# Kernel tuning notes

Hardware: AMD Instinct MI355X
Metric: run time of the kernel (lower is better)

## Reference

```python
import jax, jax.numpy as jnp
import numpy as np

VOCAB = 250002
UNUSED = np.array([0, 2, 1, 3])  # cls, eos, pad, unk token ids for XLM-R tokenizer
TEMP = 0.02
H = 1024


def _normalize(x, axis=-1):
    n = jnp.sqrt(jnp.sum(x * x, axis=axis, keepdims=True))
    return x / jnp.maximum(n, 1e-12)


def _sparse_embedding(hidden, ids, sparse_w, sparse_b):
    # token_weights = relu(Linear(H,1)(hidden)) -> [B, L]
    tw = jax.nn.relu(jnp.einsum('blh,h->bl', hidden, sparse_w) + sparse_b)
    B = hidden.shape[0]
    # torch: scatter into [B, L, V] then max over L; since tw >= 0 and base is 0,
    # this equals a scatter-max into [B, V] (avoids the huge [B,L,V] intermediate).
    emb = jnp.zeros((B, VOCAB), tw.dtype)
    emb = emb.at[jnp.arange(B)[:, None], ids].max(tw)
    emb = emb.at[:, UNUSED].set(0.0)
    return emb


def _colbert_embedding(hidden, mask, colbert_w, colbert_b):
    # Linear on tokens 1: (drop CLS), mask, then L2-normalize
    v = jnp.einsum('blh,dh->bld', hidden[:, 1:], colbert_w) + colbert_b
    v = v * mask[:, 1:, None]
    return _normalize(v)


def setup_inputs() -> dict:
    key = jax.random.key(0)
    ks = jax.random.split(key, 8)
    return {
        'q_hidden': jax.random.normal(ks[0], (8, 128, H), jnp.float32),
        'p_hidden': jax.random.normal(ks[1], (64, 512, H), jnp.float32),
        'q_mask': jnp.ones((8, 128), jnp.float32),
        'p_mask': jnp.ones((64, 512), jnp.float32),
        'q_ids': jax.random.randint(ks[2], (8, 128), 0, VOCAB),
        'p_ids': jax.random.randint(ks[3], (64, 512), 0, VOCAB),
        'colbert_w': jax.random.normal(ks[4], (H, H), jnp.float32) * 0.02,
        'colbert_b': jnp.zeros((H,), jnp.float32),
        'sparse_w': jax.random.normal(ks[5], (H,), jnp.float32) * 0.02,
        'sparse_b': jnp.zeros((), jnp.float32),
    }


def reference(q_hidden, p_hidden, q_mask, p_mask, q_ids, p_ids,
              colbert_w, colbert_b, sparse_w, sparse_b):
    # dense: cls pooling + normalize
    q_dense = _normalize(q_hidden[:, 0])
    p_dense = _normalize(p_hidden[:, 0])
    dense_scores = (q_dense @ p_dense.T) / TEMP  # [Bq, Bp]

    # sparse: relu-weighted vocab scatter-max
    q_sparse = _sparse_embedding(q_hidden, q_ids, sparse_w, sparse_b)
    p_sparse = _sparse_embedding(p_hidden, p_ids, sparse_w, sparse_b)
    sparse_scores = (q_sparse @ p_sparse.T) / TEMP  # [Bq, Bp]

    # colbert: late-interaction maxsim
    q_col = _colbert_embedding(q_hidden, q_mask, colbert_w, colbert_b)  # [Bq, Lq-1, H]
    p_col = _colbert_embedding(p_hidden, p_mask, colbert_w, colbert_b)  # [Bp, Lp-1, H]
    token_scores = jnp.einsum('qin,pjn->qipj', q_col, p_col)  # [Bq, Lq-1, Bp, Lp-1]
    colbert_scores = token_scores.max(-1).sum(1)
    colbert_scores = colbert_scores / q_mask[:, 1:].sum(-1, keepdims=True)
    colbert_scores = colbert_scores / TEMP  # [Bq, Bp]

    return dense_scores, sparse_scores, colbert_scores
```

## Files before the change

### kernel.cpp

```cpp
#include <hip/hip_runtime.h>
#include <hip/hip_bf16.h>


typedef __bf16 bf16x8 __attribute__((ext_vector_type(8)));
typedef float floatx4 __attribute__((ext_vector_type(4)));
typedef unsigned short ushort8v __attribute__((ext_vector_type(8)));

#define TEMP 0.02f

__device__ __forceinline__ unsigned short f2bf(float f) {
    unsigned u = __float_as_uint(f);
    unsigned r = (u + 0x7FFFu + ((u >> 16) & 1u)) >> 16;
    return (unsigned short)r;
}
__device__ __forceinline__ unsigned encf(float f) {
    unsigned u = __float_as_uint(f);
    return (u & 0x80000000u) ? ~u : (u | 0x80000000u);
}
__device__ __forceinline__ float decf(unsigned u) {
    return __uint_as_float((u & 0x80000000u) ? (u & 0x7FFFFFFFu) : ~u);
}

__device__ __forceinline__ void async_load16(void* lds, const void* g) {
    __builtin_amdgcn_global_load_lds(
        (__attribute__((address_space(1))) void*)g,
        (__attribute__((address_space(3))) void*)lds,
        16, 0, 0);
}

__global__ void conv_zero_tw(const float* __restrict__ qh, const float* __restrict__ ph,
                             const float* __restrict__ wsrc, unsigned short* __restrict__ dst,
                             const float* __restrict__ sw, const float* __restrict__ sb,
                             float* __restrict__ tw, unsigned* __restrict__ zbase)
{
    __shared__ float red[4];
    int b = blockIdx.x, t = threadIdx.x;
    if (b < 388) zbase[b * 256 + t] = 0u;
    int r0 = b * 2;
    const float* src;
    bool do_tw = true;
    if (r0 < 1024)       { src = qh   + (size_t)r0 * 1024; }
    else if (r0 < 33792) { src = ph   + (size_t)(r0 - 1024) * 1024; }
    else                 { src = wsrc + (size_t)(r0 - 33792) * 1024; do_tw = false; }
    const float4* s4 = (const float4*)src;
    float4 a = s4[t * 2], c = s4[t * 2 + 1];
    ushort8v o;
    o[0] = f2bf(a.x); o[1] = f2bf(a.y); o[2] = f2bf(a.z); o[3] = f2bf(a.w);
    o[4] = f2bf(c.x); o[5] = f2bf(c.y); o[6] = f2bf(c.z); o[7] = f2bf(c.w);
    ((ushort8v*)dst)[(size_t)b * 256 + t] = o;
    if (do_tw) {
        const float4* w4 = (const float4*)sw;
        int wi = (t & 127) * 2;
        float4 wa = w4[wi], wc = w4[wi + 1];
        float acc = a.x * wa.x + a.y * wa.y + a.z * wa.z + a.w * wa.w
                  + c.x * wc.x + c.y * wc.y + c.z * wc.z + c.w * wc.w;
        #pragma unroll
        for (int s = 32; s; s >>= 1) acc += __shfl_down(acc, s, 64);
        if ((t & 63) == 0) red[t >> 6] = acc;
        __syncthreads();
        if (t == 0)   tw[r0]     = fmaxf(red[0] + red[1] + sb[0], 0.0f);
        if (t == 128) tw[r0 + 1] = fmaxf(red[2] + red[3] + sb[0], 0.0f);
    }
}

__global__ void canon_all(const int* __restrict__ q_ids, const int* __restrict__ p_ids,
                          const float* __restrict__ tw,
                          float* __restrict__ eff_q, float* __restrict__ eff_p)
{
    __shared__ int   sid[512];
    __shared__ float stw[512];
    int b = blockIdx.x, t = threadIdx.x;
    const int* ids; const float* twr; float* eff; int L, chunk;
    if (b < 8) {
        L = 128; chunk = 0;
        ids = q_ids + b * 128; twr = tw + b * 128; eff = eff_q + b * 128;
    } else {
        int pr = (b - 8) >> 1; chunk = (b - 8) & 1; L = 512;
        ids = p_ids + pr * 512; twr = tw + 1024 + pr * 512; eff = eff_p + pr * 512;
    }
    for (int l = t; l < L; l += 256) { sid[l] = ids[l]; stw[l] = twr[l]; }
    __syncthreads();
    int l = chunk * 256 + t;
    if (l < L) {
        int id = sid[l];
        float wv = stw[l];
        bool kill = (id < 4);
        #pragma unroll 8
        for (int m = 0; m < L; ++m) {
            int idm = sid[m];
            float wm = stw[m];
            bool beats = (idm == id) & (m != l) & ((wm > wv) | ((wm == wv) & (m < l)));
            kill = kill | beats;
        }
        eff[l] = kill ? 0.0f : wv;
    }
}

template<int MODE>
__global__ __launch_bounds__(256, 2)
void gemm_bt(const unsigned short* __restrict__ A,
             const unsigned short* __restrict__ B,
             const float* __restrict__ bias,
             unsigned short* __restrict__ C,
             unsigned* __restrict__ Mbuf,
             float* __restrict__ normsq,
             const float* __restrict__ p_mask,
             int nTails, int N, int K,
             const float* __restrict__ qh, const float* __restrict__ ph,
             const int* __restrict__ q_ids, const int* __restrict__ p_ids,
             const float* __restrict__ eff_q, const float* __restrict__ eff_p,
             float* __restrict__ out)
{
    __shared__ unsigned short smA[128 * 64];
    __shared__ unsigned short smB[128 * 64];
    const int tid  = threadIdx.x;

    if (MODE == 0 && (int)blockIdx.x < nTails) {
        int pair = (int)blockIdx.x;
        int qb = pair >> 6, pb = pair & 63;
        char* lds = (char*)smA;
        int*   qid = (int*)lds;
        float* qef = (float*)(lds + 512);
        int*   pid = (int*)(lds + 1024);
        float* pef = (float*)(lds + 3072);
        float* redD = (float*)(lds + 5120);
        float* redS = (float*)(lds + 5184);
        int t = tid;
        if (t < 128) { qid[t] = q_ids[qb * 128 + t]; qef[t] = eff_q[qb * 128 + t]; }
        for (int m = t; m < 512; m += 256) { pid[m] = p_ids[pb * 512 + m]; pef[m] = eff_p[pb * 512 + m]; }
        const float4* q4 = (const float4*)(qh + (size_t)qb * 128 * 1024);
        const float4* p4 = (const float4*)(ph + (size_t)pb * 512 * 1024);
        float4 a = q4[t], b = p4[t];
        float dot = a.x * b.x + a.y * b.y + a.z * b.z + a.w * b.w;
        float nq  = a.x * a.x + a.y * a.y + a.z * a.z + a.w * a.w;
        float np  = b.x * b.x + b.y * b.y + b.z * b.z + b.w * b.w;
        #pragma unroll
        for (int sh = 32; sh; sh >>= 1) {
            dot += __shfl_down(dot, sh, 64);
            nq  += __shfl_down(nq, sh, 64);
            np  += __shfl_down(np, sh, 64);
        }
        if ((t & 63) == 0) { int w = t >> 6; redD[w] = dot; redD[4 + w] = nq; redD[8 + w] = np; }
        __syncthreads();
        if (t == 0) {
            float d = redD[0] + redD[1] + redD[2] + redD[3];
            float n1 = redD[4] + redD[5] + redD[6] + redD[7];
            float n2 = redD[8] + redD[9] + redD[10] + redD[11];
            out[qb * 64 + pb] = d / (fmaxf(sqrtf(n1), 1e-12f) * fmaxf(sqrtf(n2), 1e-12f)) / TEMP;
        }
        float s = 0.0f;
        for (int idx = t; idx < 128 * 512; idx += 256) {
            int l = idx >> 9, m = idx & 511;
            if (qid[l] == pid[m]) s += qef[l] * pef[m];
        }
        #pragma unroll
        for (int sh = 32; sh; sh >>= 1) s += __shfl_down(s, sh, 64);
        if ((t & 63) == 0) redS[t >> 6] = s;
        __syncthreads();
        if (t == 0) out[512 + qb * 64 + pb] = (redS[0] + redS[1] + redS[2] + redS[3]) / TEMP;
        return;
    }

    const int lane = tid & 63;
    const int w    = tid >> 6;
    const int wm   = w >> 1, wn = w & 1;
    const int quad = lane >> 4, m16 = lane & 15;

    const int id = (int)blockIdx.x - nTails;
    const int g  = id >> 6;
    const int s8 = id & 7;
    const int k8 = (id >> 3) & 7;
    const int rowTile = (MODE == 0) ? (g * 8 + s8) : k8;
    const int colTile = (MODE == 0) ? k8 : (g * 8 + s8);
    const int rowBase = rowTile * 128;
    const int colBase = colTile * 128;

    const int sr = lane >> 2;
    const int scg = (lane & 3) ^ ((lane >> 3) & 3);
    const unsigned short* aG0 = A + (long long)(rowBase + w * 16 + sr) * K + scg * 8;
    const unsigned short* aG1 = aG0 + 64LL * K;
    const unsigned short* bG0 = B + (long long)(colBase + w * 16 + sr) * K + scg * 8;
    const unsigned short* bG1 = bG0 + 64LL * K;
    unsigned short* lA0 = smA + w * 512;
    unsigned short* lA1 = smA + (w + 4) * 512;
    unsigned short* lB0 = smB + w * 512;
    unsigned short* lB1 = smB + (w + 4) * 512;

    const int fragOff = (m16 * 4 + (quad ^ ((m16 >> 1) & 3))) * 8;

    floatx4 acc[4][4] = {};

    for (int k0 = 0; k0 < K; k0 += 64) {
        async_load16(lA0,        aG0 + k0);
        async_load16(lA0 + 4096, aG0 + k0 + 32);
        async_load16(lA1,        aG1 + k0);
        async_load16(lA1 + 4096, aG1 + k0 + 32);
        async_load16(lB0,        bG0 + k0);
        async_load16(lB0 + 4096, bG0 + k0 + 32);
        async_load16(lB1,        bG1 + k0);
        async_load16(lB1 + 4096, bG1 + k0 + 32);
        __syncthreads();
        #pragma unroll
        for (int h = 0; h < 2; ++h) {
            bf16x8 af[4], bfr[4];
            #pragma unroll
            for (int f = 0; f < 4; ++f) {
                af[f]  = *(const bf16x8*)(smA + h * 4096 + (wm * 4 + f) * 512 + fragOff);
                bfr[f] = *(const bf16x8*)(smB + h * 4096 + (wn * 4 + f) * 512 + fragOff);
            }
            #pragma unroll
            for (int i = 0; i < 4; ++i)
                #pragma unroll
                for (int j = 0; j < 4; ++j)
                    acc[i][j] = __builtin_amdgcn_mfma_f32_16x16x32_bf16(af[i], bfr[j], acc[i][j], 0, 0, 0);
        }
        __syncthreads();
    }

    if (MODE == 0) {
        float bcol[4];
        #pragma unroll
        for (int j = 0; j < 4; ++j) bcol[j] = bias[colBase + wn * 64 + j * 16 + m16];
        #pragma unroll
        for (int i = 0; i < 4; ++i) {
            int row0 = rowBase + wm * 64 + i * 16 + quad * 4;
            #pragma unroll
            for (int r = 0; r < 4; ++r) {
                float sq = 0.0f;
                #pragma unroll
                for (int j = 0; j < 4; ++j) {
                    int col = colBase + wn * 64 + j * 16 + m16;
                    float val = acc[i][j][r] + bcol[j];
                    C[(long long)(row0 + r) * N + col] = f2bf(val);
                    sq += val * val;
                }
                #pragma unroll
                for (int s = 1; s < 16; s <<= 1) sq += __shfl_xor(sq, s, 64);
                if (m16 == 0) atomicAdd(&normsq[row0 + r], sq);
            }
        }
    } else {
        const int pb = colBase >> 9;
        float pfac[4];
        #pragma unroll
        for (int j = 0; j < 4; ++j) {
            int colg = colBase + wn * 64 + j * 16 + m16;
            float pm = p_mask[colg];
            float pn = sqrtf(normsq[1024 + colg]);
            pfac[j] = pm / fmaxf(pn * pm, 1e-12f);
        }
        #pragma unroll
        for (int i = 0; i < 4; ++i) {
            #pragma unroll
            for (int r = 0; r < 4; ++r) {
                float mx = -3.0e38f;
                #pragma unroll
                for (int j = 0; j < 4; ++j) {
                    int colg = colBase + wn * 64 + j * 16 + m16;
                    float v = acc[i][j][r] * pfac[j];
                    if ((colg & 511) == 0) v = -3.0e38f;
                    mx = fmaxf(mx, v);
                }
                #pragma unroll
                for (int s = 1; s < 16; s <<= 1) mx = fmaxf(mx, __shfl_xor(mx, s, 64));
                if (m16 == 0) {
                    int row = rowBase + wm * 64 + i * 16 + quad * 4 + r;
                    atomicMax(&Mbuf[row * 64 + pb], encf(mx));
                }
            }
        }
    }
}

__global__ void colbert_reduce_k(const unsigned* __restrict__ Mbuf,
                                 const float* __restrict__ q_mask,
                                 const float* __restrict__ normsq,
                                 float* __restrict__ out)
{
    int pair = blockIdx.x * 4 + (threadIdx.x >> 6);
    int lane = threadIdx.x & 63;
    int qb = pair >> 6, pb = pair & 63;
    float s = 0.0f, msum = 0.0f;
    for (int i = 1 + lane; i < 128; i += 64) {
        float qm = q_mask[qb * 128 + i];
        float qn = sqrtf(normsq[qb * 128 + i]);
        float qfac = qm / fmaxf(qn * qm, 1e-12f);
        s += decf(Mbuf[(qb * 128 + i) * 64 + pb]) * qfac;
        msum += qm;
    }
    #pragma unroll
    for (int sh = 32; sh; sh >>= 1) {
        s += __shfl_down(s, sh, 64);
        msum += __shfl_down(msum, sh, 64);
    }
    if (lane == 0) out[1024 + qb * 64 + pb] = s / msum / TEMP;
}

extern "C" void kernel_launch(void* const* d_in, const int* in_sizes, int n_in,
                              void* d_out, int out_size, void* d_ws, size_t ws_size,
                              hipStream_t stream)
{
    const float* q_hidden = (const float*)d_in[0];
    const float* p_hidden = (const float*)d_in[1];
    const float* q_mask   = (const float*)d_in[2];
    const float* p_mask   = (const float*)d_in[3];
    const int*   q_ids    = (const int*)d_in[4];
    const int*   p_ids    = (const int*)d_in[5];
    const float* colbert_w = (const float*)d_in[6];
    const float* colbert_b = (const float*)d_in[7];
    const float* sparse_w  = (const float*)d_in[8];
    const float* sparse_b  = (const float*)d_in[9];
    float* out = (float*)d_out;

    char* ws = (char*)d_ws;
    size_t off = 0;
    auto carve = [&](size_t bytes) { char* p = ws + off; off += (bytes + 255) & ~(size_t)255; return p; };
    unsigned short* qhb  = (unsigned short*)carve((size_t)1024 * 1024 * 2);
    unsigned short* phb  = (unsigned short*)carve((size_t)32768 * 1024 * 2);
    unsigned short* Wb   = (unsigned short*)carve((size_t)1024 * 1024 * 2);
    unsigned short* qv   = (unsigned short*)carve((size_t)1024 * 1024 * 2);
    unsigned short* pv   = (unsigned short*)carve((size_t)32768 * 1024 * 2);
    unsigned* Mbuf  = (unsigned*)carve((size_t)1024 * 64 * 4);
    float*    normsq = (float*)carve((size_t)33792 * 4);
    float*    tw    = (float*)carve((size_t)33792 * 4);
    float*    eff_q = (float*)carve(1024 * 4);
    float*    eff_p = (float*)carve(32768 * 4);
    (void)phb; (void)Wb; (void)pv;

    conv_zero_tw<<<17408, 256, 0, stream>>>(q_hidden, p_hidden, colbert_w, qhb,
                                            sparse_w, sparse_b, tw, Mbuf);

    canon_all<<<136, 256, 0, stream>>>(q_ids, p_ids, tw, eff_q, eff_p);

    gemm_bt<0><<<512 + 2112, 256, 0, stream>>>(
        qhb, Wb, colbert_b, qv, nullptr, normsq, nullptr, 512, 1024, 1024,
        q_hidden, p_hidden, q_ids, p_ids, eff_q, eff_p, out);

    gemm_bt<1><<<2048, 256, 0, stream>>>(
        qv, pv, nullptr, nullptr, Mbuf, normsq, p_mask, 0, 32768, 1024,
        nullptr, nullptr, nullptr, nullptr, nullptr, nullptr, nullptr);

    colbert_reduce_k<<<128, 256, 0, stream>>>(Mbuf, q_mask, normsq, out);
}
```

Measured before the change: 403.3 us.

## Store ColBERT projections in FP8 and run maxsim GEMM with FP8 MFMA

The projection GEMM now writes its token vectors as FP8 e4m3 instead of bf16. The maxsim GEMM reads them reinterpreted as ushort with K halved, and splits each bf16x8 fragment into two 8-byte FP8 operands for the fp8 MFMA. This halves memory traffic and LDS footprint per K step for the dominant Q x P token GEMM, and uses higher-throughput FP8 matrix instructions. The cost is lower precision in the maxsim scores, which may exceed tolerance. Norms are still computed in fp32 before quantization.

```diff
diff --git a/kernel.cpp b/kernel.cpp
--- a/kernel.cpp
+++ b/kernel.cpp
@@ -1,5 +1,6 @@
 #include <hip/hip_runtime.h>
 #include <hip/hip_bf16.h>
+#include <hip/hip_fp8.h>
 
 
 typedef __bf16 bf16x8 __attribute__((ext_vector_type(8)));
@@ -12,6 +13,10 @@
     unsigned u = __float_as_uint(f);
     unsigned r = (u + 0x7FFFu + ((u >> 16) & 1u)) >> 16;
     return (unsigned short)r;
+}
+__device__ __forceinline__ unsigned char f2e4m3(float f) {
+    __hip_fp8_e4m3 h(f);
+    return (unsigned char)h.__x;
 }
 __device__ __forceinline__ unsigned encf(float f) {
     unsigned u = __float_as_uint(f);
@@ -101,7 +106,7 @@
 void gemm_bt(const unsigned short* __restrict__ A,
              const unsigned short* __restrict__ B,
              const float* __restrict__ bias,
-             unsigned short* __restrict__ C,
+             unsigned char* __restrict__ C,
              unsigned* __restrict__ Mbuf,
              float* __restrict__ normsq,
              const float* __restrict__ p_mask,
@@ -208,11 +213,24 @@
                 af[f]  = *(const bf16x8*)(smA + h * 4096 + (wm * 4 + f) * 512 + fragOff);
                 bfr[f] = *(const bf16x8*)(smB + h * 4096 + (wn * 4 + f) * 512 + fragOff);
             }
-            #pragma unroll
-            for (int i = 0; i < 4; ++i)
-                #pragma unroll
-                for (int j = 0; j < 4; ++j)
-                    acc[i][j] = __builtin_amdgcn_mfma_f32_16x16x32_bf16(af[i], bfr[j], acc[i][j], 0, 0, 0);
+            if (MODE == 0) {
+                #pragma unroll
+                for (int i = 0; i < 4; ++i)
+                    #pragma unroll
+                    for (int j = 0; j < 4; ++j)
+                        acc[i][j] = __builtin_amdgcn_mfma_f32_16x16x32_bf16(af[i], bfr[j], acc[i][j], 0, 0, 0);
+            } else {
+                #pragma unroll
+                for (int i = 0; i < 4; ++i) {
+                    const long* ai = (const long*)&af[i];
+                    #pragma unroll
+                    for (int j = 0; j < 4; ++j) {
+                        const long* bj = (const long*)&bfr[j];
+                        acc[i][j] = __builtin_amdgcn_mfma_f32_16x16x32_fp8_fp8(ai[0], bj[0], acc[i][j], 0, 0, 0);
+                        acc[i][j] = __builtin_amdgcn_mfma_f32_16x16x32_fp8_fp8(ai[1], bj[1], acc[i][j], 0, 0, 0);
+                    }
+                }
+            }
         }
         __syncthreads();
     }
@@ -231,7 +249,7 @@
                 for (int j = 0; j < 4; ++j) {
                     int col = colBase + wn * 64 + j * 16 + m16;
                     float val = acc[i][j][r] + bcol[j];
-                    C[(long long)(row0 + r) * N + col] = f2bf(val);
+                    C[(long long)(row0 + r) * N + col] = f2e4m3(val);
                     sq += val * val;
                 }
                 #pragma unroll
@@ -318,14 +336,14 @@
     unsigned short* qhb  = (unsigned short*)carve((size_t)1024 * 1024 * 2);
     unsigned short* phb  = (unsigned short*)carve((size_t)32768 * 1024 * 2);
     unsigned short* Wb   = (unsigned short*)carve((size_t)1024 * 1024 * 2);
-    unsigned short* qv   = (unsigned short*)carve((size_t)1024 * 1024 * 2);
-    unsigned short* pv   = (unsigned short*)carve((size_t)32768 * 1024 * 2);
+    unsigned char*  qv8  = (unsigned char*)carve((size_t)1024 * 1024);
+    unsigned char*  pv8  = (unsigned char*)carve((size_t)32768 * 1024);
     unsigned* Mbuf  = (unsigned*)carve((size_t)1024 * 64 * 4);
     float*    normsq = (float*)carve((size_t)33792 * 4);
     float*    tw    = (float*)carve((size_t)33792 * 4);
     float*    eff_q = (float*)carve(1024 * 4);
     float*    eff_p = (float*)carve(32768 * 4);
-    (void)phb; (void)Wb; (void)pv;
+    (void)phb; (void)Wb; (void)pv8;
 
     conv_zero_tw<<<17408, 256, 0, stream>>>(q_hidden, p_hidden, colbert_w, qhb,
                                             sparse_w, sparse_b, tw, Mbuf);
@@ -333,11 +351,12 @@
     canon_all<<<136, 256, 0, stream>>>(q_ids, p_ids, tw, eff_q, eff_p);
 
     gemm_bt<0><<<512 + 2112, 256, 0, stream>>>(
-        qhb, Wb, colbert_b, qv, nullptr, normsq, nullptr, 512, 1024, 1024,
+        qhb, Wb, colbert_b, qv8, nullptr, normsq, nullptr, 512, 1024, 1024,
         q_hidden, p_hidden, q_ids, p_ids, eff_q, eff_p, out);
 
     gemm_bt<1><<<2048, 256, 0, stream>>>(
-        qv, pv, nullptr, nullptr, Mbuf, normsq, p_mask, 0, 32768, 1024,
+        (const unsigned short*)qv8, (const unsigned short*)pv8,
+        nullptr, nullptr, Mbuf, normsq, p_mask, 0, 32768, 512,
         nullptr, nullptr, nullptr, nullptr, nullptr, nullptr, nullptr);
 
     colbert_reduce_k<<<128, 256, 0, stream>>>(Mbuf, q_mask, normsq, out);
```

Measured after the change: 378.2 us. 1.07x faster.
